# Optimization experiments

Measured on AMD Instinct MI355X. Metric: run time of the kernel, lower is better.

The kernel has to match this reference:

```python
import jax, jax.numpy as jnp
import numpy as np

N_GRAPHS = 500
NODES_PER_GRAPH = 100
EDGES_PER_GRAPH = 800
IN_DIM = 64
HIDDEN = 128
RATIO = 0.8
N = N_GRAPHS * NODES_PER_GRAPH          # 50000 nodes
E = N_GRAPHS * EDGES_PER_GRAPH          # 400000 edges
K = int(RATIO * EDGES_PER_GRAPH)        # 640 causal edges kept per graph


def _lin(key, fan_in, fan_out):
    return jax.random.normal(key, (fan_in, fan_out), jnp.float32) / float(np.sqrt(fan_in))


def setup_inputs() -> dict:
    key = jax.random.key(0)
    ks = jax.random.split(key, 20)
    x = jax.random.normal(ks[0], (N, IN_DIM), jnp.float32)
    src = jax.random.randint(ks[1], (N_GRAPHS, EDGES_PER_GRAPH), 0, NODES_PER_GRAPH)
    dst = jax.random.randint(ks[2], (N_GRAPHS, EDGES_PER_GRAPH), 0, NODES_PER_GRAPH)
    offs = (jnp.arange(N_GRAPHS) * NODES_PER_GRAPH)[:, None]
    edge_index = jnp.stack([(src + offs).reshape(-1), (dst + offs).reshape(-1)]).astype(jnp.int32)
    edge_attr = jax.random.normal(ks[3], (E,), jnp.float32)
    batch_idx = jnp.repeat(jnp.arange(N_GRAPHS, dtype=jnp.int32), NODES_PER_GRAPH)
    inp = dict(x=x, edge_index=edge_index, edge_attr=edge_attr, batch_idx=batch_idx)
    # LEConv1 (in_dim -> hidden): lin1 (bias), lin2 (no bias), lin3 (bias)
    inp['c1_w1'] = _lin(ks[4], IN_DIM, HIDDEN); inp['c1_b1'] = jnp.zeros((HIDDEN,), jnp.float32)
    inp['c1_w2'] = _lin(ks[5], IN_DIM, HIDDEN)
    inp['c1_w3'] = _lin(ks[6], IN_DIM, HIDDEN); inp['c1_b3'] = jnp.zeros((HIDDEN,), jnp.float32)
    # LEConv2 (hidden -> hidden)
    inp['c2_w1'] = _lin(ks[7], HIDDEN, HIDDEN); inp['c2_b1'] = jnp.zeros((HIDDEN,), jnp.float32)
    inp['c2_w2'] = _lin(ks[8], HIDDEN, HIDDEN)
    inp['c2_w3'] = _lin(ks[9], HIDDEN, HIDDEN); inp['c2_b3'] = jnp.zeros((HIDDEN,), jnp.float32)
    # edge-score MLP: Linear(2h,4h) -> ReLU -> Linear(4h,1)
    inp['mlp_w1'] = _lin(ks[10], 2 * HIDDEN, 4 * HIDDEN); inp['mlp_b1'] = jnp.zeros((4 * HIDDEN,), jnp.float32)
    inp['mlp_w2'] = _lin(ks[11], 4 * HIDDEN, 1); inp['mlp_b2'] = jnp.zeros((1,), jnp.float32)
    return inp


def leconv(x, edge_index, ew, w1, b1, w2, w3, b3):
    # PyG LEConv: out_i = sum_{j->i} w_ji * (lin1(x_j) - lin2(x_i)) + lin3(x_i)
    a = x @ w1 + b1
    b = x @ w2
    src, dst = edge_index[0], edge_index[1]
    msg = (a[src] - b[dst]) * ew[:, None]
    agg = jax.ops.segment_sum(msg, dst, num_segments=x.shape[0])
    return agg + x @ w3 + b3


def relabel(x, edge_index, batch):
    # fixed-size unique: pads with sentinel n; x/batch padded with a dummy row
    n = x.shape[0]
    sub = jnp.unique(edge_index.reshape(-1), size=n, fill_value=n)
    x_pad = jnp.concatenate([x, jnp.zeros((1, x.shape[1]), x.dtype)], axis=0)
    b_pad = jnp.concatenate([batch, jnp.full((1,), -1, batch.dtype)])
    node_idx = jnp.full((n + 1,), -1, jnp.int32).at[sub].set(jnp.arange(n, dtype=jnp.int32))
    return x_pad[sub], node_idx[edge_index], b_pad[sub]


def _forward(x, edge_index, edge_attr, batch_idx,
             c1_w1, c1_b1, c1_w2, c1_w3, c1_b3,
             c2_w1, c2_b1, c2_w2, c2_w3, c2_b3,
             mlp_w1, mlp_b1, mlp_w2, mlp_b2):
    ew = edge_attr.reshape(-1)
    h = jax.nn.relu(leconv(x, edge_index, ew, c1_w1, c1_b1, c1_w2, c1_w3, c1_b3))
    h = leconv(h, edge_index, ew, c2_w1, c2_b1, c2_w2, c2_w3, c2_b3)
    src, dst = edge_index[0], edge_index[1]
    edge_rep = jnp.concatenate([h[src], h[dst]], axis=-1)                  # [E, 2h]
    edge_score = (jax.nn.relu(edge_rep @ mlp_w1 + mlp_b1) @ mlp_w2 + mlp_b2).reshape(-1)
    # per-graph top-k split (equal-size graphs -> static [B, E_g] view)
    scores = edge_score.reshape(N_GRAPHS, EDGES_PER_GRAPH)
    order = jnp.argsort(-scores, axis=1)
    offs = (jnp.arange(N_GRAPHS) * EDGES_PER_GRAPH)[:, None]
    idx_res = (order[:, :K] + offs).reshape(-1)
    idx_drop = (order[:, K:] + offs).reshape(-1)
    c_ei = edge_index[:, idx_res]
    f_ei = edge_index[:, idx_drop]
    c_w = edge_score[idx_res]
    f_w = -edge_score[idx_drop]
    c_attr = edge_attr[idx_res]
    f_attr = edge_attr[idx_drop]
    c_x, c_ei2, c_b = relabel(h, c_ei, batch_idx)
    f_x, f_ei2, f_b = relabel(h, f_ei, batch_idx)
    return (c_x, c_ei2, c_attr, c_w, c_b, f_x, f_ei2, f_attr, f_w, f_b, edge_score)


def reference(x, edge_index, edge_attr, batch_idx,
              c1_w1, c1_b1, c1_w2, c1_w3, c1_b3,
              c2_w1, c2_b1, c2_w2, c2_w3, c2_b3,
              mlp_w1, mlp_b1, mlp_w2, mlp_b2):
    return _forward(x, edge_index, edge_attr, batch_idx,
                    c1_w1, c1_b1, c1_w2, c1_w3, c1_b3,
                    c2_w1, c2_b1, c2_w2, c2_w3, c2_b3,
                    mlp_w1, mlp_b1, mlp_w2, mlp_b2)
```

## Files before the change

### kernel.cpp

```cpp
#include <hip/hip_runtime.h>

#define NG 500
#define NPG 100
#define EPG 800
#define INDIM 64
#define HID 128
#define ETOT (NG*EPG)
#define NTOT (NG*NPG)
#define KKEEP 640
#define KDROP 160
#define MAXDEG 64

#define OFF_CX    0u
#define OFF_CEI   6400000u
#define OFF_CATTR 7040000u
#define OFF_CW    7360000u
#define OFF_CB    7680000u
#define OFF_FX    7730000u
#define OFF_FEI   14130000u
#define OFF_FATTR 14290000u
#define OFF_FW    14370000u
#define OFF_FB    14450000u
#define OFF_ES    14500000u

__global__ __launch_bounds__(128) void prep_kernel(
    const int* __restrict__ ei, const float* __restrict__ ea,
    float2* __restrict__ elist2, int* __restrict__ ecnt, float* __restrict__ sdeg)
{
  __shared__ unsigned char esrcL[EPG];
  __shared__ unsigned char edstL[EPG];
  __shared__ float ewvL[EPG];
  const int g = blockIdx.x, t = threadIdx.x;
  const int nb = g * NPG;
  for (int e = t; e < EPG; e += 128) {
    int ge = g * EPG + e;
    esrcL[e] = (unsigned char)(ei[ge] - nb);
    edstL[e] = (unsigned char)(ei[ETOT + ge] - nb);
    ewvL[e] = ea[ge];
  }
  __syncthreads();
  if (t < NPG) {
    int cnt = 0; float s = 0.f;
    float2* lp = elist2 + (size_t)(nb + t) * MAXDEG;
    for (int e = 0; e < EPG; e++) {
      if ((int)edstL[e] == t) {
        if (cnt < MAXDEG) lp[cnt] = make_float2(ewvL[e], __int_as_float((int)esrcL[e]));
        cnt++; s += ewvL[e];
      }
    }
    ecnt[nb + t] = cnt < MAXDEG ? cnt : MAXDEG;
    sdeg[nb + t] = s;
  }
}

template<int K>
__global__ __launch_bounds__(512) void preagg_kernel(
    const float* __restrict__ xin, const float2* __restrict__ elist2,
    const int* __restrict__ ecnt, float* __restrict__ y)
{
  __shared__ float xt[NPG][K];
  const int g = blockIdx.x, t = threadIdx.x;
  const int nb = g * NPG;
  for (int i = t; i < NPG * K / 4; i += 512)
    ((float4*)xt)[i] = ((const float4*)(xin + (size_t)nb * K))[i];
  __syncthreads();
  const int c = t % K, grp = t / K;
  const int NGRP = 512 / K;
  for (int d = grp; d < NPG; d += NGRP) {
    const int cn = ecnt[nb + d];
    const float2* lp = elist2 + (size_t)(nb + d) * MAXDEG;
    float acc = 0.f;
    for (int j = 0; j < cn; j++) {
      float2 p = lp[j];
      acc += p.x * xt[__float_as_int(p.y)][c];
    }
    y[(size_t)(nb + d) * K + c] = acc;
  }
}

template<int K, bool RELU>
__global__ __launch_bounds__(256) void conv_gemm_kernel(
    const float* __restrict__ y, const float* __restrict__ xin, const float* __restrict__ sdeg,
    const float* __restrict__ w1, const float* __restrict__ w2, const float* __restrict__ w3,
    const float* __restrict__ b1, const float* __restrict__ b3,
    float* __restrict__ hout)
{
  __shared__ float wl[64][HID];
  const int t = threadIdx.x;
  const int m0 = blockIdx.x * 128;
  const int tc = t % 16;
  const int tr = t / 16;
  float acc[8][8];
#pragma unroll
  for (int i = 0; i < 8; i++)
#pragma unroll
    for (int j = 0; j < 8; j++) acc[i][j] = 0.f;

  int rowc[8]; float sdv[8];
#pragma unroll
  for (int i = 0; i < 8; i++) {
    int r = m0 + tr * 8 + i;
    rowc[i] = r < NTOT ? r : NTOT - 1;
    sdv[i] = sdeg[rowc[i]];
  }
  const int NCH = (3 * K) / 64;
  for (int ch = 0; ch < NCH; ++ch) {
    __syncthreads();
    for (int i = t; i < 64 * HID / 4; i += 256) {
      int kk = i / 32, q = i % 32;
      int kr = ch * 64 + kk;
      int seg = kr / K; int sr = kr % K;
      const float* wp = seg == 0 ? w1 : (seg == 1 ? w3 : w2);
      float4 v = *(const float4*)(wp + (size_t)sr * HID + q * 4);
      if (seg == 2) { v.x = -v.x; v.y = -v.y; v.z = -v.z; v.w = -v.w; }
      *(float4*)&wl[kk][q * 4] = v;
    }
    __syncthreads();
    const int seg = (ch * 64) / K;
    const int kb = (ch * 64) % K;
    for (int k4 = 0; k4 < 16; ++k4) {
      float4 a4[8];
#pragma unroll
      for (int i = 0; i < 8; i++) {
        const float* src = (seg == 0 ? y : xin) + (size_t)rowc[i] * K + kb + k4 * 4;
        float4 v = *(const float4*)src;
        if (seg == 2) { float s = sdv[i]; v.x *= s; v.y *= s; v.z *= s; v.w *= s; }
        a4[i] = v;
      }
#pragma unroll
      for (int kk = 0; kk < 4; kk++) {
        float wv0[4], wv1[4];
        *(float4*)wv0 = *(const float4*)&wl[k4 * 4 + kk][tc * 4];
        *(float4*)wv1 = *(const float4*)&wl[k4 * 4 + kk][64 + tc * 4];
#pragma unroll
        for (int i = 0; i < 8; i++) {
          const float av = (&a4[i].x)[kk];
#pragma unroll
          for (int j = 0; j < 4; j++) {
            acc[i][j]     += av * wv0[j];
            acc[i][4 + j] += av * wv1[j];
          }
        }
      }
    }
  }
#pragma unroll
  for (int i = 0; i < 8; i++) {
    const int r = m0 + tr * 8 + i;
    if (r < NTOT) {
      float4 o0, o1;
#pragma unroll
      for (int j = 0; j < 4; j++) {
        float c0 = acc[i][j]     + sdv[i] * b1[tc * 4 + j]      + b3[tc * 4 + j];
        float c1 = acc[i][4 + j] + sdv[i] * b1[64 + tc * 4 + j] + b3[64 + tc * 4 + j];
        if (RELU) { c0 = fmaxf(c0, 0.f); c1 = fmaxf(c1, 0.f); }
        (&o0.x)[j] = c0; (&o1.x)[j] = c1;
      }
      float* op = hout + (size_t)r * HID;
      *(float4*)(op + tc * 4) = o0;
      *(float4*)(op + 64 + tc * 4) = o1;
    }
  }
}

__global__ __launch_bounds__(256) void pq_gemm_kernel(
    const float* __restrict__ h2, const float* __restrict__ mw1, const float* __restrict__ mb1,
    float* __restrict__ PQ)
{
  __shared__ float wl[64][HID];
  const int t = threadIdx.x;
  const int m0 = blockIdx.x * 128;
  const int n0 = blockIdx.y * 128;
  const int tc = t % 16, tr = t / 16;
  const int basek = (n0 >= 512) ? HID : 0;
  const int cbase = n0 & 511;

  float acc[8][8];
#pragma unroll
  for (int i = 0; i < 8; i++) {
#pragma unroll
    for (int j = 0; j < 4; j++) {
      acc[i][j]     = (basek == 0) ? mb1[n0 + tc * 4 + j] : 0.f;
      acc[i][4 + j] = (basek == 0) ? mb1[n0 + 64 + tc * 4 + j] : 0.f;
    }
  }
  int rowc[8];
#pragma unroll
  for (int i = 0; i < 8; i++) {
    int r = m0 + tr * 8 + i;
    rowc[i] = r < NTOT ? r : NTOT - 1;
  }

  for (int ch = 0; ch < 2; ++ch) {
    __syncthreads();
    for (int i = t; i < 64 * 32; i += 256) {
      int kk = i / 32, q = i % 32;
      *(float4*)&wl[kk][q * 4] =
          *(const float4*)(mw1 + (size_t)(basek + ch * 64 + kk) * 512 + cbase + q * 4);
    }
    __syncthreads();
    for (int k4 = 0; k4 < 16; ++k4) {
      float4 a4[8];
#pragma unroll
      for (int i = 0; i < 8; i++)
        a4[i] = *(const float4*)(h2 + (size_t)rowc[i] * HID + ch * 64 + k4 * 4);
#pragma unroll
      for (int kk = 0; kk < 4; kk++) {
        float wv0[4], wv1[4];
        *(float4*)wv0 = *(const float4*)&wl[k4 * 4 + kk][tc * 4];
        *(float4*)wv1 = *(const float4*)&wl[k4 * 4 + kk][64 + tc * 4];
#pragma unroll
        for (int i = 0; i < 8; i++) {
          const float av = (&a4[i].x)[kk];
#pragma unroll
          for (int j = 0; j < 4; j++) {
            acc[i][j]     += av * wv0[j];
            acc[i][4 + j] += av * wv1[j];
          }
        }
      }
    }
  }
#pragma unroll
  for (int i = 0; i < 8; i++) {
    const int r = m0 + tr * 8 + i;
    if (r < NTOT) {
      float* op = PQ + (size_t)r * 1024 + n0;
      *(float4*)(op + tc * 4)      = *(float4*)&acc[i][0];
      *(float4*)(op + 64 + tc * 4) = *(float4*)&acc[i][4];
    }
  }
}

__global__ __launch_bounds__(256) void edge_sort_kernel(
    const float* __restrict__ PQ, const int* __restrict__ ei,
    const float* __restrict__ mw2, const float* __restrict__ mb2,
    float* __restrict__ scores_ws, float* __restrict__ out_es,
    int* __restrict__ keptEid, int* __restrict__ dropEid,
    int* __restrict__ cLocal, int* __restrict__ fLocal,
    int* __restrict__ cCount, int* __restrict__ fCount)
{
  __shared__ float Pl[NPG][68];
  __shared__ float Ql[NPG][68];
  __shared__ float w2l[64];
  __shared__ unsigned char esrcL[EPG];
  __shared__ unsigned char edstL[EPG];
  __shared__ unsigned long long keys[1024];
  __shared__ int cpres[NPG];
  __shared__ int fpres[NPG];

  const int g = blockIdx.x, t = threadIdx.x;
  const int nb = g * NPG;

  for (int e = t; e < EPG; e += 256) {
    int ge = g * EPG + e;
    esrcL[e] = (unsigned char)(ei[ge] - nb);
    edstL[e] = (unsigned char)(ei[ETOT + ge] - nb);
  }
  for (int i = t; i < NPG; i += 256) { cpres[i] = 0; fpres[i] = 0; }
  __syncthreads();

  int sl[4], dl[4];
#pragma unroll
  for (int m = 0; m < 4; m++) {
    const int e = t + 256 * m;
    const int ec = e < EPG ? e : 0;
    sl[m] = esrcL[ec]; dl[m] = edstL[ec];
  }
  double accd[4];
#pragma unroll
  for (int m = 0; m < 4; m++) accd[m] = 0.;

  for (int ch = 0; ch < 8; ++ch) {
    __syncthreads();
    for (int i = t; i < NPG * 16; i += 256) {
      const int r = i >> 4, q = i & 15;
      const float* src = PQ + (size_t)(nb + r) * 1024 + ch * 64 + q * 4;
      *(float4*)&Pl[r][q * 4] = *(const float4*)src;
      *(float4*)&Ql[r][q * 4] = *(const float4*)(src + 512);
    }
    if (t < 16) *(float4*)&w2l[t * 4] = *(const float4*)(mw2 + ch * 64 + t * 4);
    __syncthreads();
#pragma unroll
    for (int m = 0; m < 4; m++) {
      double aa = 0.;
      for (int j4 = 0; j4 < 16; ++j4) {
        const float4 p = *(const float4*)&Pl[sl[m]][j4 * 4];
        const float4 q = *(const float4*)&Ql[dl[m]][j4 * 4];
        const float4 w = *(const float4*)&w2l[j4 * 4];
        const float s = fmaxf(p.x + q.x, 0.f) * w.x + fmaxf(p.y + q.y, 0.f) * w.y
                      + fmaxf(p.z + q.z, 0.f) * w.z + fmaxf(p.w + q.w, 0.f) * w.w;
        aa += (double)s;
      }
      accd[m] += aa;
    }
  }

  const double b2v = (double)mb2[0];
#pragma unroll
  for (int m = 0; m < 4; m++) {
    const int e = t + 256 * m;
    if (e < EPG) {
      const float sc = (float)(accd[m] + b2v);
      const int ge = g * EPG + e;
      scores_ws[ge] = sc; out_es[ge] = sc;
      const unsigned int bb = __float_as_uint(sc);
      const unsigned int mm = (bb & 0x80000000u) ? (~bb) : (bb | 0x80000000u);
      keys[e] = ((unsigned long long)(~mm) << 32) | (unsigned int)e;
    }
  }
  if (t >= 32) keys[t + 768] = 0xFFFFFFFFFFFFFFFFull;
  __syncthreads();

  for (int k = 2; k <= 1024; k <<= 1) {
    for (int j = k >> 1; j > 0; j >>= 1) {
      for (int i = t; i < 1024; i += 256) {
        const int l = i ^ j;
        if (l > i) {
          const bool up = ((i & k) == 0);
          const unsigned long long va = keys[i], vb = keys[l];
          if ((va > vb) == up) { keys[i] = vb; keys[l] = va; }
        }
      }
      __syncthreads();
    }
  }

  for (int r = t; r < EPG; r += 256) {
    const int el = (int)(unsigned int)keys[r];
    const int ge = g * EPG + el;
    const int s0 = esrcL[el], d0 = edstL[el];
    if (r < KKEEP) {
      keptEid[g * KKEEP + r] = ge;
      cpres[s0] = 1; cpres[d0] = 1;
    } else {
      dropEid[g * KDROP + (r - KKEEP)] = ge;
      fpres[s0] = 1; fpres[d0] = 1;
    }
  }
  __syncthreads();

  if (t == 0) {
    int cc = 0;
    for (int v = 0; v < NPG; v++) { const int pr = cpres[v]; cLocal[nb + v] = pr ? cc : -1; cc += pr; }
    cCount[g] = cc;
  }
  if (t == 64) {
    int fc = 0;
    for (int v = 0; v < NPG; v++) { const int pr = fpres[v]; fLocal[nb + v] = pr ? fc : -1; fc += pr; }
    fCount[g] = fc;
  }
}

__global__ __launch_bounds__(512) void offsets_kernel(
    const int* __restrict__ cCount, const int* __restrict__ fCount,
    int* __restrict__ cOff, int* __restrict__ fOff)
{
  __shared__ int sc[512];
  __shared__ int sf[512];
  const int t = threadIdx.x;
  const int c0 = (t < NG) ? cCount[t] : 0;
  const int f0 = (t < NG) ? fCount[t] : 0;
  sc[t] = c0; sf[t] = f0;
  __syncthreads();
  for (int off = 1; off < 512; off <<= 1) {
    const int ac = (t >= off) ? sc[t - off] : 0;
    const int af = (t >= off) ? sf[t - off] : 0;
    __syncthreads();
    sc[t] += ac; sf[t] += af;
    __syncthreads();
  }
  if (t < NG) { cOff[t] = sc[t] - c0; fOff[t] = sf[t] - f0; }
  if (t == NG - 1) { cOff[NG] = sc[t]; fOff[NG] = sf[t]; }
}

__global__ __launch_bounds__(256) void scatter_kernel(
    const float* __restrict__ h2, const int* __restrict__ cLocal, const int* __restrict__ fLocal,
    const int* __restrict__ cOff, const int* __restrict__ fOff,
    int* __restrict__ nodeIdxC, int* __restrict__ nodeIdxF, float* __restrict__ out)
{
  const int tid = blockIdx.x * 256 + threadIdx.x;
  if (tid >= 2 * NTOT * 32) return;
  const int side = tid >= NTOT * 32 ? 1 : 0;
  const int rem = tid - side * NTOT * 32;
  const int v = rem >> 5, q = rem & 31;
  const int loc = side ? fLocal[v] : cLocal[v];
  if (loc < 0) return;
  const int g = v / NPG;
  const int pos = (side ? fOff[g] : cOff[g]) + loc;
  const float4* srcv = (const float4*)(h2 + (size_t)v * HID);
  float4* dstv = (float4*)(out + (side ? OFF_FX : OFF_CX) + (size_t)pos * HID);
  dstv[q] = srcv[q];
  if (q == 0) {
    (side ? nodeIdxF : nodeIdxC)[v] = pos;
    out[(side ? OFF_FB : OFF_CB) + pos] = (float)g;
  }
}

__global__ __launch_bounds__(256) void fill_kernel(
    const int* __restrict__ cOff, const int* __restrict__ fOff, float* __restrict__ out)
{
  const int tid = blockIdx.x * 256 + threadIdx.x;
  if (tid >= 2 * NTOT * 32) return;
  const int side = tid >= NTOT * 32 ? 1 : 0;
  const int rem = tid - side * NTOT * 32;
  const int r = rem >> 5, q = rem & 31;
  const int total = side ? fOff[NG] : cOff[NG];
  if (r < total) return;
  float4 z; z.x = 0.f; z.y = 0.f; z.z = 0.f; z.w = 0.f;
  ((float4*)(out + (side ? OFF_FX : OFF_CX)))[(size_t)r * 32 + q] = z;
  if (q == 0) out[(side ? OFF_FB : OFF_CB) + r] = -1.0f;
}

__global__ __launch_bounds__(256) void edgeout_kernel(
    const int* __restrict__ ei, const float* __restrict__ ea, const float* __restrict__ scores,
    const int* __restrict__ keptEid, const int* __restrict__ dropEid,
    const int* __restrict__ nodeIdxC, const int* __restrict__ nodeIdxF, float* __restrict__ out)
{
  const int tid = blockIdx.x * 256 + threadIdx.x;
  if (tid >= ETOT) return;
  if (tid < NG * KKEEP) {
    const int ge = keptEid[tid];
    out[OFF_CEI + tid] = (float)nodeIdxC[ei[ge]];
    out[OFF_CEI + 320000 + tid] = (float)nodeIdxC[ei[ETOT + ge]];
    out[OFF_CATTR + tid] = ea[ge];
    out[OFF_CW + tid] = scores[ge];
  } else {
    const int i = tid - NG * KKEEP;
    const int ge = dropEid[i];
    out[OFF_FEI + i] = (float)nodeIdxF[ei[ge]];
    out[OFF_FEI + 80000 + i] = (float)nodeIdxF[ei[ETOT + ge]];
    out[OFF_FATTR + i] = ea[ge];
    out[OFF_FW + i] = -scores[ge];
  }
}

extern "C" void kernel_launch(void* const* d_in, const int* in_sizes, int n_in,
                              void* d_out, int out_size, void* d_ws, size_t ws_size,
                              hipStream_t stream) {
  const float* x    = (const float*)d_in[0];
  const int*   ei   = (const int*)d_in[1];
  const float* ea   = (const float*)d_in[2];
  const float* c1w1 = (const float*)d_in[4];
  const float* c1b1 = (const float*)d_in[5];
  const float* c1w2 = (const float*)d_in[6];
  const float* c1w3 = (const float*)d_in[7];
  const float* c1b3 = (const float*)d_in[8];
  const float* c2w1 = (const float*)d_in[9];
  const float* c2b1 = (const float*)d_in[10];
  const float* c2w2 = (const float*)d_in[11];
  const float* c2w3 = (const float*)d_in[12];
  const float* c2b3 = (const float*)d_in[13];
  const float* mw1  = (const float*)d_in[14];
  const float* mb1  = (const float*)d_in[15];
  const float* mw2  = (const float*)d_in[16];
  const float* mb2  = (const float*)d_in[17];
  float* out = (float*)d_out;

  char* p = (char*)d_ws;
  auto carve = [&](size_t bytes) { void* r = (void*)p; p += (bytes + 255) & ~(size_t)255; return r; };
  float* h2      = (float*)carve((size_t)NTOT * HID * 4);
  float* scores  = (float*)carve((size_t)ETOT * 4);
  int* keptEid   = (int*)carve((size_t)NG * KKEEP * 4);
  int* dropEid   = (int*)carve((size_t)NG * KDROP * 4);
  int* cLocal    = (int*)carve((size_t)NTOT * 4);
  int* fLocal    = (int*)carve((size_t)NTOT * 4);
  int* cCount    = (int*)carve((size_t)NG * 4);
  int* fCount    = (int*)carve((size_t)NG * 4);
  int* cOff      = (int*)carve((size_t)(NG + 1) * 4);
  int* fOff      = (int*)carve((size_t)(NG + 1) * 4);
  int* nodeIdxC  = (int*)carve((size_t)NTOT * 4);
  int* nodeIdxF  = (int*)carve((size_t)NTOT * 4);
  char* ub = (char*)carve((size_t)NTOT * 1024 * 4);
  float* PQ      = (float*)ub;
  float* h1      = (float*)ub;
  float* ybuf    = (float*)(ub + (size_t)NTOT * HID * 4);
  float2* elist2 = (float2*)(ub + (size_t)2 * NTOT * HID * 4);
  int* ecnt      = (int*)(ub + (size_t)2 * NTOT * HID * 4 + (size_t)NTOT * MAXDEG * 8);
  float* sdeg    = (float*)(ub + (size_t)2 * NTOT * HID * 4 + (size_t)NTOT * MAXDEG * 8 + (size_t)NTOT * 4);

  const int MT = (NTOT + 127) / 128;

  prep_kernel<<<NG, 128, 0, stream>>>(ei, ea, elist2, ecnt, sdeg);
  preagg_kernel<INDIM><<<NG, 512, 0, stream>>>(x, elist2, ecnt, ybuf);
  conv_gemm_kernel<INDIM, true><<<MT, 256, 0, stream>>>(ybuf, x, sdeg, c1w1, c1w2, c1w3, c1b1, c1b3, h1);
  preagg_kernel<HID><<<NG, 512, 0, stream>>>(h1, elist2, ecnt, ybuf);
  conv_gemm_kernel<HID, false><<<MT, 256, 0, stream>>>(ybuf, h1, sdeg, c2w1, c2w2, c2w3, c2b1, c2b3, h2);
  dim3 pqgrid(MT, 8);
  pq_gemm_kernel<<<pqgrid, 256, 0, stream>>>(h2, mw1, mb1, PQ);
  edge_sort_kernel<<<NG, 256, 0, stream>>>(PQ, ei, mw2, mb2, scores, out + OFF_ES,
                                           keptEid, dropEid, cLocal, fLocal, cCount, fCount);
  offsets_kernel<<<1, 512, 0, stream>>>(cCount, fCount, cOff, fOff);
  const int sc_threads = 2 * NTOT * 32;
  scatter_kernel<<<(sc_threads + 255) / 256, 256, 0, stream>>>(h2, cLocal, fLocal, cOff, fOff, nodeIdxC, nodeIdxF, out);
  fill_kernel<<<(sc_threads + 255) / 256, 256, 0, stream>>>(cOff, fOff, out);
  edgeout_kernel<<<(ETOT + 255) / 256, 256, 0, stream>>>(ei, ea, scores, keptEid, dropEid, nodeIdxC, nodeIdxF, out);
}
```

Baseline: 833.1 us.

## Stage GEMM A-tiles in shared memory and trim edge-score staging

```diff
diff --git a/kernel.cpp b/kernel.cpp
--- a/kernel.cpp
+++ b/kernel.cpp
@@ -86,6 +86,7 @@
     float* __restrict__ hout)
 {
   __shared__ float wl[64][HID];
+  __shared__ float al[128][68];
   const int t = threadIdx.x;
   const int m0 = blockIdx.x * 128;
   const int tc = t % 16;
@@ -106,27 +107,33 @@
   const int NCH = (3 * K) / 64;
   for (int ch = 0; ch < NCH; ++ch) {
     __syncthreads();
+    const int seg = (ch * 64) / K;
+    const int kb = (ch * 64) % K;
     for (int i = t; i < 64 * HID / 4; i += 256) {
       int kk = i / 32, q = i % 32;
       int kr = ch * 64 + kk;
-      int seg = kr / K; int sr = kr % K;
+      int sr = kr % K;
       const float* wp = seg == 0 ? w1 : (seg == 1 ? w3 : w2);
       float4 v = *(const float4*)(wp + (size_t)sr * HID + q * 4);
       if (seg == 2) { v.x = -v.x; v.y = -v.y; v.z = -v.z; v.w = -v.w; }
       *(float4*)&wl[kk][q * 4] = v;
     }
-    __syncthreads();
-    const int seg = (ch * 64) / K;
-    const int kb = (ch * 64) % K;
+    {
+      const float* abase = (seg == 0 ? y : xin);
+      for (int i = t; i < 128 * 16; i += 256) {
+        int r = i / 16, q = i % 16;
+        int gr = m0 + r; if (gr >= NTOT) gr = NTOT - 1;
+        float4 v = *(const float4*)(abase + (size_t)gr * K + kb + q * 4);
+        if (seg == 2) { float s = sdeg[gr]; v.x *= s; v.y *= s; v.z *= s; v.w *= s; }
+        *(float4*)&al[r][q * 4] = v;
+      }
+    }
+    __syncthreads();
     for (int k4 = 0; k4 < 16; ++k4) {
       float4 a4[8];
 #pragma unroll
-      for (int i = 0; i < 8; i++) {
-        const float* src = (seg == 0 ? y : xin) + (size_t)rowc[i] * K + kb + k4 * 4;
-        float4 v = *(const float4*)src;
-        if (seg == 2) { float s = sdv[i]; v.x *= s; v.y *= s; v.z *= s; v.w *= s; }
-        a4[i] = v;
-      }
+      for (int i = 0; i < 8; i++)
+        a4[i] = *(const float4*)&al[tr * 8 + i][k4 * 4];
 #pragma unroll
       for (int kk = 0; kk < 4; kk++) {
         float wv0[4], wv1[4];
@@ -168,6 +175,7 @@
     float* __restrict__ PQ)
 {
   __shared__ float wl[64][HID];
+  __shared__ float al[128][68];
   const int t = threadIdx.x;
   const int m0 = blockIdx.x * 128;
   const int n0 = blockIdx.y * 128;
@@ -177,19 +185,9 @@
 
   float acc[8][8];
 #pragma unroll
-  for (int i = 0; i < 8; i++) {
-#pragma unroll
-    for (int j = 0; j < 4; j++) {
-      acc[i][j]     = (basek == 0) ? mb1[n0 + tc * 4 + j] : 0.f;
-      acc[i][4 + j] = (basek == 0) ? mb1[n0 + 64 + tc * 4 + j] : 0.f;
-    }
-  }
-  int rowc[8];
-#pragma unroll
-  for (int i = 0; i < 8; i++) {
-    int r = m0 + tr * 8 + i;
-    rowc[i] = r < NTOT ? r : NTOT - 1;
-  }
+  for (int i = 0; i < 8; i++)
+#pragma unroll
+    for (int j = 0; j < 8; j++) acc[i][j] = 0.f;
 
   for (int ch = 0; ch < 2; ++ch) {
     __syncthreads();
@@ -198,12 +196,17 @@
       *(float4*)&wl[kk][q * 4] =
           *(const float4*)(mw1 + (size_t)(basek + ch * 64 + kk) * 512 + cbase + q * 4);
     }
+    for (int i = t; i < 128 * 16; i += 256) {
+      int r = i / 16, q = i % 16;
+      int gr = m0 + r; if (gr >= NTOT) gr = NTOT - 1;
+      *(float4*)&al[r][q * 4] = *(const float4*)(h2 + (size_t)gr * HID + ch * 64 + q * 4);
+    }
     __syncthreads();
     for (int k4 = 0; k4 < 16; ++k4) {
       float4 a4[8];
 #pragma unroll
       for (int i = 0; i < 8; i++)
-        a4[i] = *(const float4*)(h2 + (size_t)rowc[i] * HID + ch * 64 + k4 * 4);
+        a4[i] = *(const float4*)&al[tr * 8 + i][k4 * 4];
 #pragma unroll
       for (int kk = 0; kk < 4; kk++) {
         float wv0[4], wv1[4];
@@ -225,9 +228,16 @@
   for (int i = 0; i < 8; i++) {
     const int r = m0 + tr * 8 + i;
     if (r < NTOT) {
+      float4 o0, o1;
+#pragma unroll
+      for (int j = 0; j < 4; j++) {
+        float c0 = acc[i][j]     + (basek == 0 ? mb1[cbase + tc * 4 + j]      : 0.f);
+        float c1 = acc[i][4 + j] + (basek == 0 ? mb1[cbase + 64 + tc * 4 + j] : 0.f);
+        (&o0.x)[j] = c0; (&o1.x)[j] = c1;
+      }
       float* op = PQ + (size_t)r * 1024 + n0;
-      *(float4*)(op + tc * 4)      = *(float4*)&acc[i][0];
-      *(float4*)(op + 64 + tc * 4) = *(float4*)&acc[i][4];
+      *(float4*)(op + tc * 4)      = o0;
+      *(float4*)(op + 64 + tc * 4) = o1;
     }
   }
 }
@@ -235,14 +245,14 @@
 __global__ __launch_bounds__(256) void edge_sort_kernel(
     const float* __restrict__ PQ, const int* __restrict__ ei,
     const float* __restrict__ mw2, const float* __restrict__ mb2,
-    float* __restrict__ scores_ws, float* __restrict__ out_es,
+    float* __restrict__ out_es,
     int* __restrict__ keptEid, int* __restrict__ dropEid,
     int* __restrict__ cLocal, int* __restrict__ fLocal,
     int* __restrict__ cCount, int* __restrict__ fCount)
 {
-  __shared__ float Pl[NPG][68];
-  __shared__ float Ql[NPG][68];
-  __shared__ float w2l[64];
+  __shared__ __align__(16) float Pl[NPG][66];
+  __shared__ __align__(16) float Ql[NPG][66];
+  __shared__ __align__(16) float w2l[512];
   __shared__ unsigned char esrcL[EPG];
   __shared__ unsigned char edstL[EPG];
   __shared__ unsigned long long keys[1024];
@@ -257,6 +267,7 @@
     esrcL[e] = (unsigned char)(ei[ge] - nb);
     edstL[e] = (unsigned char)(ei[ETOT + ge] - nb);
   }
+  for (int i = t; i < 128; i += 256) *(float4*)&w2l[i * 4] = *(const float4*)(mw2 + i * 4);
   for (int i = t; i < NPG; i += 256) { cpres[i] = 0; fpres[i] = 0; }
   __syncthreads();
 
@@ -273,23 +284,24 @@
 
   for (int ch = 0; ch < 8; ++ch) {
     __syncthreads();
-    for (int i = t; i < NPG * 16; i += 256) {
-      const int r = i >> 4, q = i & 15;
-      const float* src = PQ + (size_t)(nb + r) * 1024 + ch * 64 + q * 4;
-      *(float4*)&Pl[r][q * 4] = *(const float4*)src;
-      *(float4*)&Ql[r][q * 4] = *(const float4*)(src + 512);
-    }
-    if (t < 16) *(float4*)&w2l[t * 4] = *(const float4*)(mw2 + ch * 64 + t * 4);
+    for (int i = t; i < NPG * 32; i += 256) {
+      const int r = i >> 5, q = i & 31;
+      const float* src = PQ + (size_t)(nb + r) * 1024 + ch * 64 + q * 2;
+      *(float2*)&Pl[r][q * 2] = *(const float2*)src;
+      *(float2*)&Ql[r][q * 2] = *(const float2*)(src + 512);
+    }
     __syncthreads();
 #pragma unroll
     for (int m = 0; m < 4; m++) {
       double aa = 0.;
       for (int j4 = 0; j4 < 16; ++j4) {
-        const float4 p = *(const float4*)&Pl[sl[m]][j4 * 4];
-        const float4 q = *(const float4*)&Ql[dl[m]][j4 * 4];
-        const float4 w = *(const float4*)&w2l[j4 * 4];
-        const float s = fmaxf(p.x + q.x, 0.f) * w.x + fmaxf(p.y + q.y, 0.f) * w.y
-                      + fmaxf(p.z + q.z, 0.f) * w.z + fmaxf(p.w + q.w, 0.f) * w.w;
+        const float2 pa = *(const float2*)&Pl[sl[m]][j4 * 4];
+        const float2 pb = *(const float2*)&Pl[sl[m]][j4 * 4 + 2];
+        const float2 qa = *(const float2*)&Ql[dl[m]][j4 * 4];
+        const float2 qb = *(const float2*)&Ql[dl[m]][j4 * 4 + 2];
+        const float4 w = *(const float4*)&w2l[ch * 64 + j4 * 4];
+        const float s = fmaxf(pa.x + qa.x, 0.f) * w.x + fmaxf(pa.y + qa.y, 0.f) * w.y
+                      + fmaxf(pb.x + qb.x, 0.f) * w.z + fmaxf(pb.y + qb.y, 0.f) * w.w;
         aa += (double)s;
       }
       accd[m] += aa;
@@ -302,8 +314,7 @@
     const int e = t + 256 * m;
     if (e < EPG) {
       const float sc = (float)(accd[m] + b2v);
-      const int ge = g * EPG + e;
-      scores_ws[ge] = sc; out_es[ge] = sc;
+      out_es[g * EPG + e] = sc;
       const unsigned int bb = __float_as_uint(sc);
       const unsigned int mm = (bb & 0x80000000u) ? (~bb) : (bb | 0x80000000u);
       keys[e] = ((unsigned long long)(~mm) << 32) | (unsigned int)e;
@@ -460,7 +471,6 @@
   char* p = (char*)d_ws;
   auto carve = [&](size_t bytes) { void* r = (void*)p; p += (bytes + 255) & ~(size_t)255; return r; };
   float* h2      = (float*)carve((size_t)NTOT * HID * 4);
-  float* scores  = (float*)carve((size_t)ETOT * 4);
   int* keptEid   = (int*)carve((size_t)NG * KKEEP * 4);
   int* dropEid   = (int*)carve((size_t)NG * KDROP * 4);
   int* cLocal    = (int*)carve((size_t)NTOT * 4);
@@ -488,11 +498,11 @@
   conv_gemm_kernel<HID, false><<<MT, 256, 0, stream>>>(ybuf, h1, sdeg, c2w1, c2w2, c2w3, c2b1, c2b3, h2);
   dim3 pqgrid(MT, 8);
   pq_gemm_kernel<<<pqgrid, 256, 0, stream>>>(h2, mw1, mb1, PQ);
-  edge_sort_kernel<<<NG, 256, 0, stream>>>(PQ, ei, mw2, mb2, scores, out + OFF_ES,
+  edge_sort_kernel<<<NG, 256, 0, stream>>>(PQ, ei, mw2, mb2, out + OFF_ES,
                                            keptEid, dropEid, cLocal, fLocal, cCount, fCount);
   offsets_kernel<<<1, 512, 0, stream>>>(cCount, fCount, cOff, fOff);
   const int sc_threads = 2 * NTOT * 32;
   scatter_kernel<<<(sc_threads + 255) / 256, 256, 0, stream>>>(h2, cLocal, fLocal, cOff, fOff, nodeIdxC, nodeIdxF, out);
   fill_kernel<<<(sc_threads + 255) / 256, 256, 0, stream>>>(cOff, fOff, out);
-  edgeout_kernel<<<(ETOT + 255) / 256, 256, 0, stream>>>(ei, ea, scores, keptEid, dropEid, nodeIdxC, nodeIdxF, out);
-}
+  edgeout_kernel<<<(ETOT + 255) / 256, 256, 0, stream>>>(ei, ea, out + OFF_ES, keptEid, dropEid, nodeIdxC, nodeIdxF, out);
+}
```

New measurement: 815.2 us. 2.1% less time.
